# Optimization experiments

Measured on AMD Instinct MI355X. Metric: run time of the kernel, lower is better.

The kernel has to match this reference:

```python
import jax, jax.numpy as jnp
import numpy as np
import math

VOCAB = 50000; D = 512; DEPTH = 6; N = 16; DCONV = 4; R = 32; DFF = 4 * D
B = 2; L = 1024

# A = -exp(A_log) with A_log = log(arange(1..N)) repeated over D  =>  A[d,n] = -(n+1)
A_CONT = -jnp.broadcast_to(jnp.arange(1.0, N + 1, dtype=jnp.float32), (D, N))


def sinusoidal(t, dim):
    half = dim // 2
    f = jnp.exp(jnp.arange(half, dtype=jnp.float32) * (-math.log(10000.0) / (half - 1)))
    e = t.astype(jnp.float32)[:, None] * f[None, :]
    return jnp.concatenate([jnp.sin(e), jnp.cos(e)], axis=-1)


def layernorm(x, g, b, eps=1e-5):
    mu = jnp.mean(x, -1, keepdims=True)
    var = jnp.mean((x - mu) ** 2, -1, keepdims=True)
    return (x - mu) * jax.lax.rsqrt(var + eps) * g + b


def ssm(x, Win, Wconv, Wdt, bdt, Dp, Wout):
    # x: [B,L,D]
    proj = x @ Win.T  # [B,L,2D+R+2N]
    xc, z, dtu, Bp, Cp = jnp.split(proj, [D, 2 * D, 2 * D + R, 2 * D + R + N], axis=-1)
    # depthwise causal conv (left pad d_conv-1 == pad both + truncate to L)
    conv = jax.lax.conv_general_dilated(
        xc.transpose(0, 2, 1), Wconv, (1,), [(DCONV - 1, 0)],
        dimension_numbers=('NCH', 'OIH', 'NCH'), feature_group_count=D)
    u = jax.nn.silu(conv.transpose(0, 2, 1))  # [B,L,D]
    dt = jax.nn.softplus(dtu @ Wdt.T + bdt)   # [B,L,D]
    At = jnp.exp(dt[..., None] * A_CONT)      # [B,L,D,N] (ZOH)
    Bu = ((At - 1.0) / (A_CONT + 1e-10)) * Bp[:, :, None, :] * u[..., None]  # [B,L,D,N]

    def step(h, xs):
        a, bu, c = xs
        h = a * h + bu                       # [B,D,N]
        return h, jnp.einsum('bn,bdn->bd', c, h)

    h0 = jnp.zeros((x.shape[0], D, N), dtype=x.dtype)
    _, ys = jax.lax.scan(step, h0, (At.transpose(1, 0, 2, 3), Bu.transpose(1, 0, 2, 3), Cp.transpose(1, 0, 2)))
    y = ys.transpose(1, 0, 2)                # [B,L,D]
    y = (y + u * Dp) * jax.nn.silu(z)
    return y @ Wout.T


def setup_inputs():
    key = jax.random.key(0)
    ks = iter(jax.random.split(key, 32))
    nrm = lambda shape: jax.random.normal(next(ks), shape, jnp.float32) * 0.02
    inp = {
        'x_t': jax.random.randint(next(ks), (B, L), 0, VOCAB + 1),
        't': jax.random.randint(next(ks), (B,), 0, 100),
        'tok_emb': nrm((VOCAB + 1, D)),
        'tmlp_w1': nrm((4 * D, D)), 'tmlp_b1': jnp.zeros((4 * D,)),
        'tmlp_w2': nrm((D, 4 * D)), 'tmlp_b2': jnp.zeros((D,)),
        'ln1_g': jnp.ones((DEPTH, D)), 'ln1_b': jnp.zeros((DEPTH, D)),
        'in_w': nrm((DEPTH, 2 * D + R + 2 * N, D)),
        'conv_w': nrm((DEPTH, D, 1, DCONV)),
        'dt_w': nrm((DEPTH, D, R)), 'dt_b': jnp.zeros((DEPTH, D)),
        'D_p': jnp.ones((DEPTH, D)),
        'out_w': nrm((DEPTH, D, D)),
        'ln2_g': jnp.ones((DEPTH, D)), 'ln2_b': jnp.zeros((DEPTH, D)),
        'mlp_w1': nrm((DEPTH, DFF, D)), 'mlp_b1': jnp.zeros((DEPTH, DFF)),
        'mlp_w2': nrm((DEPTH, D, DFF)), 'mlp_b2': jnp.zeros((DEPTH, D)),
        'lno_g': jnp.ones((D,)), 'lno_b': jnp.zeros((D,)),
        'head_w': nrm((VOCAB, D)), 'head_b': jnp.zeros((VOCAB,)),
    }
    return inp


def reference(x_t, t, tok_emb, tmlp_w1, tmlp_b1, tmlp_w2, tmlp_b2,
              ln1_g, ln1_b, in_w, conv_w, dt_w, dt_b, D_p, out_w,
              ln2_g, ln2_b, mlp_w1, mlp_b1, mlp_w2, mlp_b2,
              lno_g, lno_b, head_w, head_b):
    te = sinusoidal(t, D)
    te = jax.nn.silu(te @ tmlp_w1.T + tmlp_b1) @ tmlp_w2.T + tmlp_b2  # [B,D]
    x = tok_emb[x_t] + te[:, None, :]                                  # [B,L,D]
    for i in range(DEPTH):
        x = x + ssm(layernorm(x, ln1_g[i], ln1_b[i]),
                    in_w[i], conv_w[i], dt_w[i], dt_b[i], D_p[i], out_w[i])
        h = layernorm(x, ln2_g[i], ln2_b[i])
        x = x + jax.nn.gelu(h @ mlp_w1[i].T + mlp_b1[i], approximate=False) @ mlp_w2[i].T + mlp_b2[i]
    x = layernorm(x, lno_g, lno_b)
    return x @ head_w.T + head_b  # [B,L,VOCAB]
```

## Files before the change

### kernel.cpp

```cpp
#include <hip/hip_runtime.h>
#include <hip/hip_bf16.h>
#include <math.h>

typedef __hip_bfloat16 bf16;
typedef short s16x8 __attribute__((ext_vector_type(8)));
typedef float f32x4 __attribute__((ext_vector_type(4)));

#define M_TOK 2048
#define DD    512
#define LSEQ  1024
#define PW    1088
#define NST   16
#define RR    32
#define DFFW  2048
#define NCH   64
#define CH    16

__device__ __forceinline__ float bf2f(bf16 v) { return __bfloat162float(v); }
__device__ __forceinline__ float siluf(float x) { return x / (1.f + expf(-x)); }

__constant__ float c_invn[NST] = {
  -1.f/1, -1.f/2, -1.f/3, -1.f/4, -1.f/5, -1.f/6, -1.f/7, -1.f/8,
  -1.f/9, -1.f/10, -1.f/11, -1.f/12, -1.f/13, -1.f/14, -1.f/15, -1.f/16 };

__global__ __launch_bounds__(256) void k_te1(
    const int* __restrict__ t, const float* __restrict__ w1, const float* __restrict__ b1,
    float* __restrict__ h1)
{
  __shared__ float semb[2][512];
  int tid = threadIdx.x;
  float t0 = (float)t[0], t1 = (float)t[1];
  {
    int k = tid;
    float f = expf((float)k * (-9.210340371976184f / 255.f));
    semb[0][k]       = sinf(t0 * f);
    semb[0][k + 256] = cosf(t0 * f);
    semb[1][k]       = sinf(t1 * f);
    semb[1][k + 256] = cosf(t1 * f);
  }
  __syncthreads();
  int wave = tid >> 6, lane = tid & 63;
  int j = blockIdx.x * 4 + wave;
  const float* wr = w1 + (size_t)j * 512;
  float s0 = 0.f, s1 = 0.f;
#pragma unroll
  for (int i = 0; i < 8; ++i) {
    int k = lane + (i << 6);
    float wv = wr[k];
    s0 += wv * semb[0][k];
    s1 += wv * semb[1][k];
  }
  for (int o = 32; o; o >>= 1) { s0 += __shfl_down(s0, o); s1 += __shfl_down(s1, o); }
  if (!lane) {
    float bv = b1[j];
    h1[j]        = siluf(s0 + bv);
    h1[2048 + j] = siluf(s1 + bv);
  }
}

__global__ __launch_bounds__(256) void k_te2(
    const float* __restrict__ h1, const float* __restrict__ w2, const float* __restrict__ b2,
    float* __restrict__ te)
{
  __shared__ float sh1[2][2048];
  int tid = threadIdx.x;
  for (int idx = tid; idx < 4096; idx += 256)
    sh1[idx >> 11][idx & 2047] = h1[idx];
  __syncthreads();
  int wave = tid >> 6, lane = tid & 63;
  int d = blockIdx.x * 4 + wave;
  const float* wr = w2 + (size_t)d * 2048;
  float s0 = 0.f, s1 = 0.f;
#pragma unroll
  for (int i = 0; i < 32; ++i) {
    int k = lane + (i << 6);
    float wv = wr[k];
    s0 += wv * sh1[0][k];
    s1 += wv * sh1[1][k];
  }
  for (int o = 32; o; o >>= 1) { s0 += __shfl_down(s0, o); s1 += __shfl_down(s1, o); }
  if (!lane) {
    float bv = b2[d];
    te[d]       = s0 + bv;
    te[512 + d] = s1 + bv;
  }
}

__global__ __launch_bounds__(256) void k_embed(
    const int* __restrict__ x_t, const float* __restrict__ tok,
    const float* __restrict__ te, float* __restrict__ x)
{
  int m = blockIdx.x;
  int b = m >> 10;
  int row = x_t[m];
  const float* src = tok + (size_t)row * DD;
  for (int d = threadIdx.x; d < DD; d += 256)
    x[(size_t)m * DD + d] = src[d] + te[b * DD + d];
}

__global__ __launch_bounds__(256) void k_layernorm(
    const float* __restrict__ x, const float* __restrict__ g, const float* __restrict__ bb,
    bf16* __restrict__ out)
{
  int m = blockIdx.x;
  const float* xr = x + (size_t)m * DD;
  float2 v = ((const float2*)xr)[threadIdx.x];
  float s = v.x + v.y, ss = v.x * v.x + v.y * v.y;
  for (int o = 32; o; o >>= 1) { s += __shfl_down(s, o); ss += __shfl_down(ss, o); }
  __shared__ float ps[4], pss[4];
  int wave = threadIdx.x >> 6, lane = threadIdx.x & 63;
  if (!lane) { ps[wave] = s; pss[wave] = ss; }
  __syncthreads();
  s = ps[0] + ps[1] + ps[2] + ps[3];
  ss = pss[0] + pss[1] + pss[2] + pss[3];
  float mu = s * (1.f / DD);
  float var = ss * (1.f / DD) - mu * mu;
  float inv = rsqrtf(var + 1e-5f);
  int d = threadIdx.x * 2;
  out[(size_t)m * DD + d]     = __float2bfloat16((v.x - mu) * inv * g[d]     + bb[d]);
  out[(size_t)m * DD + d + 1] = __float2bfloat16((v.y - mu) * inv * g[d + 1] + bb[d + 1]);
}

__global__ __launch_bounds__(256) void k_conv_dt(
    const float* __restrict__ proj, const float* __restrict__ convw,
    const float* __restrict__ dtw, const float* __restrict__ dtb,
    float* __restrict__ u, float* __restrict__ dt)
{
  int m = blockIdx.x >> 1;
  int d = ((blockIdx.x & 1) << 8) + threadIdx.x;
  int b = m >> 10, l = m & 1023;
  __shared__ float dtu[RR];
  if (threadIdx.x < RR) dtu[threadIdx.x] = proj[(size_t)m * PW + 2 * DD + threadIdx.x];
  __syncthreads();
  float c = 0.f;
#pragma unroll
  for (int j = 0; j < 4; ++j) {
    int ll = l - 3 + j;
    if (ll >= 0) c += proj[(size_t)(b * LSEQ + ll) * PW + d] * convw[d * 4 + j];
  }
  u[(size_t)m * DD + d] = siluf(c);
  float s = dtb[d];
  const float* wr = dtw + (size_t)d * RR;
#pragma unroll
  for (int r = 0; r < RR; ++r) s += dtu[r] * wr[r];
  dt[(size_t)m * DD + d] = (s > 0.f) ? (s + log1pf(expf(-s))) : log1pf(expf(s));
}

__global__ __launch_bounds__(128) void k_scan1(
    const float* __restrict__ proj, const float* __restrict__ u,
    const float* __restrict__ dt, float* __restrict__ yloc,
    float* __restrict__ Ebuf, float* __restrict__ Aprod, float* __restrict__ hend)
{
  int d = (blockIdx.x << 7) + threadIdx.x;
  int c = blockIdx.y, b = blockIdx.z;
  int m0 = b * LSEQ + c * CH;
  __shared__ float sBC[CH][32];
  for (int idx = threadIdx.x; idx < CH * 32; idx += 128)
    sBC[idx >> 5][idx & 31] = proj[(size_t)(m0 + (idx >> 5)) * PW + 2 * DD + RR + (idx & 31)];
  __syncthreads();
  float h[NST];
#pragma unroll
  for (int n = 0; n < NST; ++n) h[n] = 0.f;
  float S = 0.f;
  for (int l = 0; l < CH; ++l) {
    size_t m = (size_t)(m0 + l);
    float dtv = dt[m * DD + d];
    float uv  = u[m * DD + d];
    float e1 = expf(-dtv);
    S += dtv;
    Ebuf[m * DD + d] = expf(-S);
    float p = 1.f, acc = 0.f;
#pragma unroll
    for (int n = 0; n < NST; ++n) {
      p *= e1;
      float bu = (p - 1.f) * c_invn[n] * sBC[l][n] * uv;
      h[n] = p * h[n] + bu;
      acc += sBC[l][16 + n] * h[n];
    }
    yloc[m * DD + d] = acc;
  }
  float Ec = expf(-S);
  float p = 1.f;
  size_t base = ((size_t)(b * NCH + c) * NST) * DD + d;
#pragma unroll
  for (int n = 0; n < NST; ++n) {
    p *= Ec;
    Aprod[base + (size_t)n * DD] = p;
    hend [base + (size_t)n * DD] = h[n];
  }
}

__global__ __launch_bounds__(256) void k_scan2(
    const float* __restrict__ Aprod, const float* __restrict__ hend, float* __restrict__ h0)
{
  int idx = blockIdx.x * 256 + threadIdx.x;
  int d = idx & 511;
  int n = (idx >> 9) & 15;
  int b = idx >> 13;
  float h = 0.f;
  for (int c = 0; c < NCH; ++c) {
    size_t o = ((size_t)((b * NCH + c) * NST + n)) * DD + d;
    h0[o] = h;
    h = Aprod[o] * h + hend[o];
  }
}

__global__ __launch_bounds__(128) void k_scan3(
    const float* __restrict__ proj, const float* __restrict__ u,
    const float* __restrict__ yloc, const float* __restrict__ Ebuf,
    const float* __restrict__ h0, const float* __restrict__ Dp, bf16* __restrict__ out)
{
  int d = (blockIdx.x << 7) + threadIdx.x;
  int c = blockIdx.y, b = blockIdx.z;
  int m0 = b * LSEQ + c * CH;
  __shared__ float sC[CH][NST];
  for (int idx = threadIdx.x; idx < CH * NST; idx += 128)
    sC[idx >> 4][idx & 15] = proj[(size_t)(m0 + (idx >> 4)) * PW + 2 * DD + RR + NST + (idx & 15)];
  __syncthreads();
  float hh[NST];
  size_t base = ((size_t)(b * NCH + c) * NST) * DD + d;
#pragma unroll
  for (int n = 0; n < NST; ++n) hh[n] = h0[base + (size_t)n * DD];
  float dpv = Dp[d];
  for (int l = 0; l < CH; ++l) {
    size_t m = (size_t)(m0 + l);
    float E = Ebuf[m * DD + d];
    float p = 1.f, corr = 0.f;
#pragma unroll
    for (int n = 0; n < NST; ++n) {
      p *= E;
      corr += sC[l][n] * p * hh[n];
    }
    float y = yloc[m * DD + d] + corr;
    float z = proj[m * PW + DD + d];
    float v = (y + u[m * DD + d] * dpv) * siluf(z);
    out[m * DD + d] = __float2bfloat16(v);
  }
}

template<int ACT, bool BF16OUT, bool RES, bool BIAS, bool TRANS>
__global__ __launch_bounds__(256) void gemm_abt(
    const bf16* __restrict__ A, const float* __restrict__ B,
    const float* __restrict__ bias, const float* __restrict__ res,
    void* __restrict__ Cout, int N, int K)
{
  __shared__ bf16 sA[128][40];
  __shared__ bf16 sB[128][40];
  int bn = (TRANS ? blockIdx.y : blockIdx.x) * 128;
  int bm = (TRANS ? blockIdx.x : blockIdx.y) * 128;
  int tid = threadIdx.x;
  int wave = tid >> 6, lane = tid & 63;
  int wm = (wave >> 1) << 6, wn = (wave & 1) << 6;
  int r = lane & 15, q = lane >> 4;
  int ldr = tid >> 2;
  int ldc = (tid & 3) << 3;

  f32x4 acc[4][4];
#pragma unroll
  for (int i = 0; i < 4; ++i)
#pragma unroll
    for (int j = 0; j < 4; ++j) acc[i][j] = (f32x4){0.f, 0.f, 0.f, 0.f};

  s16x8 pa[2];
  f32x4 pb[2][2];
#define GLOAD(k0)                                                              \
  {                                                                            \
    _Pragma("unroll")                                                          \
    for (int h = 0; h < 2; ++h) {                                              \
      int row = ldr + (h << 6);                                                \
      pa[h] = *(const s16x8*)(A + (size_t)(bm + row) * K + (k0) + ldc);        \
      int nrow = bn + row;                                                     \
      if (nrow < N) {                                                          \
        const float* src = B + (size_t)nrow * K + (k0) + ldc;                  \
        pb[h][0] = *(const f32x4*)src;                                         \
        pb[h][1] = *(const f32x4*)(src + 4);                                   \
      } else {                                                                 \
        pb[h][0] = (f32x4){0.f,0.f,0.f,0.f};                                   \
        pb[h][1] = (f32x4){0.f,0.f,0.f,0.f};                                   \
      }                                                                        \
    }                                                                          \
  }

  GLOAD(0);
  for (int k0 = 0; k0 < K; k0 += 32) {
#pragma unroll
    for (int h = 0; h < 2; ++h) {
      int row = ldr + (h << 6);
      *(s16x8*)&sA[row][ldc] = pa[h];
      bf16* dst = &sB[row][ldc];
      dst[0] = __float2bfloat16(pb[h][0][0]); dst[1] = __float2bfloat16(pb[h][0][1]);
      dst[2] = __float2bfloat16(pb[h][0][2]); dst[3] = __float2bfloat16(pb[h][0][3]);
      dst[4] = __float2bfloat16(pb[h][1][0]); dst[5] = __float2bfloat16(pb[h][1][1]);
      dst[6] = __float2bfloat16(pb[h][1][2]); dst[7] = __float2bfloat16(pb[h][1][3]);
    }
    __syncthreads();
    if (k0 + 32 < K) GLOAD(k0 + 32);
    s16x8 af[4], bg[4];
#pragma unroll
    for (int i = 0; i < 4; ++i) af[i] = *(s16x8*)&sA[wm + i * 16 + r][q << 3];
#pragma unroll
    for (int j = 0; j < 4; ++j) bg[j] = *(s16x8*)&sB[wn + j * 16 + r][q << 3];
#pragma unroll
    for (int i = 0; i < 4; ++i)
#pragma unroll
      for (int j = 0; j < 4; ++j)
        acc[i][j] = __builtin_amdgcn_mfma_f32_16x16x32_bf16(af[i], bg[j], acc[i][j], 0, 0, 0);
    __syncthreads();
  }
#undef GLOAD

#pragma unroll
  for (int i = 0; i < 4; ++i)
#pragma unroll
    for (int j = 0; j < 4; ++j) {
      int n = bn + wn + j * 16 + r;
      if (n >= N) continue;
#pragma unroll
      for (int e = 0; e < 4; ++e) {
        int m = bm + wm + i * 16 + (q << 2) + e;
        float v = acc[i][j][e];
        if (BIAS) v += bias[n];
        if (ACT == 1) v = 0.5f * v * (1.f + erff(v * 0.70710678118f));
        if (RES) v += res[(size_t)m * N + n];
        if (BF16OUT) ((bf16*)Cout)[(size_t)m * N + n] = __float2bfloat16(v);
        else         ((float*)Cout)[(size_t)m * N + n] = v;
      }
    }
}

template<int ACT, bool BF16OUT, bool RES, bool BIAS>
__global__ __launch_bounds__(256) void gemm64(
    const bf16* __restrict__ A, const float* __restrict__ B,
    const float* __restrict__ bias, const float* __restrict__ res,
    void* __restrict__ Cout, int N, int K)
{
  __shared__ bf16 sA[64][40];
  __shared__ bf16 sB[64][40];
  int bn = blockIdx.x * 64;
  int bm = blockIdx.y * 64;
  int tid = threadIdx.x;
  int wave = tid >> 6, lane = tid & 63;
  int wm = (wave >> 1) << 5, wn = (wave & 1) << 5;
  int r = lane & 15, q = lane >> 4;
  int ldr = tid >> 2;
  int ldc = (tid & 3) << 3;

  f32x4 acc[2][2];
#pragma unroll
  for (int i = 0; i < 2; ++i)
#pragma unroll
    for (int j = 0; j < 2; ++j) acc[i][j] = (f32x4){0.f, 0.f, 0.f, 0.f};

  s16x8 pa;
  f32x4 pb[2];
#define GLOAD64(k0)                                                            \
  {                                                                            \
    pa = *(const s16x8*)(A + (size_t)(bm + ldr) * K + (k0) + ldc);             \
    const float* src = B + (size_t)(bn + ldr) * K + (k0) + ldc;                \
    pb[0] = *(const f32x4*)src;                                                \
    pb[1] = *(const f32x4*)(src + 4);                                          \
  }

  GLOAD64(0);
  for (int k0 = 0; k0 < K; k0 += 32) {
    *(s16x8*)&sA[ldr][ldc] = pa;
    {
      bf16* dst = &sB[ldr][ldc];
      dst[0] = __float2bfloat16(pb[0][0]); dst[1] = __float2bfloat16(pb[0][1]);
      dst[2] = __float2bfloat16(pb[0][2]); dst[3] = __float2bfloat16(pb[0][3]);
      dst[4] = __float2bfloat16(pb[1][0]); dst[5] = __float2bfloat16(pb[1][1]);
      dst[6] = __float2bfloat16(pb[1][2]); dst[7] = __float2bfloat16(pb[1][3]);
    }
    __syncthreads();
    if (k0 + 32 < K) GLOAD64(k0 + 32);
    s16x8 af[2], bg[2];
#pragma unroll
    for (int i = 0; i < 2; ++i) af[i] = *(s16x8*)&sA[wm + i * 16 + r][q << 3];
#pragma unroll
    for (int j = 0; j < 2; ++j) bg[j] = *(s16x8*)&sB[wn + j * 16 + r][q << 3];
#pragma unroll
    for (int i = 0; i < 2; ++i)
#pragma unroll
      for (int j = 0; j < 2; ++j)
        acc[i][j] = __builtin_amdgcn_mfma_f32_16x16x32_bf16(af[i], bg[j], acc[i][j], 0, 0, 0);
    __syncthreads();
  }
#undef GLOAD64

#pragma unroll
  for (int i = 0; i < 2; ++i)
#pragma unroll
    for (int j = 0; j < 2; ++j) {
      int n = bn + wn + j * 16 + r;
#pragma unroll
      for (int e = 0; e < 4; ++e) {
        int m = bm + wm + i * 16 + (q << 2) + e;
        float v = acc[i][j][e];
        if (BIAS) v += bias[n];
        if (ACT == 1) v = 0.5f * v * (1.f + erff(v * 0.70710678118f));
        if (RES) v += res[(size_t)m * N + n];
        if (BF16OUT) ((bf16*)Cout)[(size_t)m * N + n] = __float2bfloat16(v);
        else         ((float*)Cout)[(size_t)m * N + n] = v;
      }
    }
}

extern "C" void kernel_launch(void* const* d_in, const int* in_sizes, int n_in,
                              void* d_out, int out_size, void* d_ws, size_t ws_size,
                              hipStream_t stream) {
  const int*   x_t     = (const int*)d_in[0];
  const int*   t       = (const int*)d_in[1];
  const float* tok_emb = (const float*)d_in[2];
  const float* tmlp_w1 = (const float*)d_in[3];
  const float* tmlp_b1 = (const float*)d_in[4];
  const float* tmlp_w2 = (const float*)d_in[5];
  const float* tmlp_b2 = (const float*)d_in[6];
  const float* ln1_g   = (const float*)d_in[7];
  const float* ln1_b   = (const float*)d_in[8];
  const float* in_w    = (const float*)d_in[9];
  const float* conv_w  = (const float*)d_in[10];
  const float* dt_w    = (const float*)d_in[11];
  const float* dt_b    = (const float*)d_in[12];
  const float* D_p     = (const float*)d_in[13];
  const float* out_w   = (const float*)d_in[14];
  const float* ln2_g   = (const float*)d_in[15];
  const float* ln2_b   = (const float*)d_in[16];
  const float* mlp_w1  = (const float*)d_in[17];
  const float* mlp_b1  = (const float*)d_in[18];
  const float* mlp_w2  = (const float*)d_in[19];
  const float* mlp_b2  = (const float*)d_in[20];
  const float* lno_g   = (const float*)d_in[21];
  const float* lno_b   = (const float*)d_in[22];
  const float* head_w  = (const float*)d_in[23];
  const float* head_b  = (const float*)d_in[24];

  char* w = (char*)d_ws;
  float* te    = (float*)w;  w += 4096;
  float* h1t   = (float*)w;  w += 16384;
  float* x     = (float*)w;  w += (size_t)M_TOK * DD * 4;
  bf16*  aIn   = (bf16*)w;   w += (size_t)M_TOK * DD * 2;
  float* proj  = (float*)w;  w += (size_t)M_TOK * PW * 4;
  float* ubuf  = (float*)w;  w += (size_t)M_TOK * DD * 4;
  float* dtbuf = (float*)w;  w += (size_t)M_TOK * DD * 4;
  float* ybuf  = (float*)w;  w += (size_t)M_TOK * DD * 4;
  float* Ebuf  = (float*)w;  w += (size_t)M_TOK * DD * 4;
  float* Aprod = (float*)w;  w += (size_t)2 * NCH * NST * DD * 4;
  float* hend  = (float*)w;  w += (size_t)2 * NCH * NST * DD * 4;
  float* h0    = (float*)w;  w += (size_t)2 * NCH * NST * DD * 4;
  bf16*  gbuf  = (bf16*)proj;

  k_te1<<<512, 256, 0, stream>>>(t, tmlp_w1, tmlp_b1, h1t);
  k_te2<<<128, 256, 0, stream>>>(h1t, tmlp_w2, tmlp_b2, te);
  k_embed<<<M_TOK, 256, 0, stream>>>(x_t, tok_emb, te, x);

  for (int i = 0; i < 6; ++i) {
    const float* inw_i  = in_w   + (size_t)i * PW * DD;
    const float* cw_i   = conv_w + (size_t)i * DD * 4;
    const float* dtw_i  = dt_w   + (size_t)i * DD * RR;
    const float* dtb_i  = dt_b   + (size_t)i * DD;
    const float* dp_i   = D_p    + (size_t)i * DD;
    const float* ow_i   = out_w  + (size_t)i * DD * DD;
    const float* m1_i   = mlp_w1 + (size_t)i * DFFW * DD;
    const float* m1b_i  = mlp_b1 + (size_t)i * DFFW;
    const float* m2_i   = mlp_w2 + (size_t)i * DD * DFFW;
    const float* m2b_i  = mlp_b2 + (size_t)i * DD;

    k_layernorm<<<M_TOK, 256, 0, stream>>>(x, ln1_g + i * DD, ln1_b + i * DD, aIn);
    gemm64<0,false,false,false><<<dim3(PW / 64, M_TOK / 64), 256, 0, stream>>>(
        aIn, inw_i, nullptr, nullptr, proj, PW, DD);
    k_conv_dt<<<M_TOK * 2, 256, 0, stream>>>(proj, cw_i, dtw_i, dtb_i, ubuf, dtbuf);
    k_scan1<<<dim3(4, NCH, 2), 128, 0, stream>>>(proj, ubuf, dtbuf, ybuf, Ebuf, Aprod, hend);
    k_scan2<<<2 * NST * DD / 256, 256, 0, stream>>>(Aprod, hend, h0);
    k_scan3<<<dim3(4, NCH, 2), 128, 0, stream>>>(proj, ubuf, ybuf, Ebuf, h0, dp_i, aIn);
    gemm64<0,false,true,false><<<dim3(DD / 64, M_TOK / 64), 256, 0, stream>>>(
        aIn, ow_i, nullptr, x, x, DD, DD);
    k_layernorm<<<M_TOK, 256, 0, stream>>>(x, ln2_g + i * DD, ln2_b + i * DD, aIn);
    gemm_abt<1,true,false,true,false><<<dim3(DFFW / 128, M_TOK / 128), 256, 0, stream>>>(
        aIn, m1_i, m1b_i, nullptr, gbuf, DFFW, DD);
    gemm64<0,false,true,true><<<dim3(DD / 64, M_TOK / 64), 256, 0, stream>>>(
        gbuf, m2_i, m2b_i, x, x, DD, DFFW);
  }

  k_layernorm<<<M_TOK, 256, 0, stream>>>(x, lno_g, lno_b, aIn);
  gemm_abt<0,false,false,true,true><<<dim3(M_TOK / 128, (50000 + 127) / 128), 256, 0, stream>>>(
      aIn, head_w, head_b, nullptr, d_out, 50000, DD);
}
```

Measured before the change: 1.272 ms.

## Swizzle head GEMM blocks, vectorize bf16 LDS stores, shrink LDS padding, use gemm64 for MLP1

The vocab head GEMM now remaps its flat block index into eight interleaved groups. The aim is that concurrently running blocks share tiles of A and B in cache. The eight scalar fp32→bf16 stores into shared memory become one packed 8-wide vector store in both GEMM kernels. Shared-memory row padding shrinks from 40 to 36 bf16, which leaves 16-byte fragment reads only 8-byte aligned and may split them or cause bank conflicts. The first MLP projection also switches from the 128×128 tile kernel to the 64×64 tile kernel, giving more blocks but less operand reuse per block.

```diff
diff --git a/kernel.cpp b/kernel.cpp
--- a/kernel.cpp
+++ b/kernel.cpp
@@ -15,9 +15,23 @@
 #define DFFW  2048
 #define NCH   64
 #define CH    16
+#define PAD   36
 
 __device__ __forceinline__ float bf2f(bf16 v) { return __bfloat162float(v); }
 __device__ __forceinline__ float siluf(float x) { return x / (1.f + expf(-x)); }
+
+__device__ __forceinline__ s16x8 cvt8(const f32x4& a, const f32x4& b) {
+  s16x8 r;
+  r[0] = (short)__bfloat16_as_ushort(__float2bfloat16(a[0]));
+  r[1] = (short)__bfloat16_as_ushort(__float2bfloat16(a[1]));
+  r[2] = (short)__bfloat16_as_ushort(__float2bfloat16(a[2]));
+  r[3] = (short)__bfloat16_as_ushort(__float2bfloat16(a[3]));
+  r[4] = (short)__bfloat16_as_ushort(__float2bfloat16(b[0]));
+  r[5] = (short)__bfloat16_as_ushort(__float2bfloat16(b[1]));
+  r[6] = (short)__bfloat16_as_ushort(__float2bfloat16(b[2]));
+  r[7] = (short)__bfloat16_as_ushort(__float2bfloat16(b[3]));
+  return r;
+}
 
 __constant__ float c_invn[NST] = {
   -1.f/1, -1.f/2, -1.f/3, -1.f/4, -1.f/5, -1.f/6, -1.f/7, -1.f/8,
@@ -238,16 +252,25 @@
   }
 }
 
-template<int ACT, bool BF16OUT, bool RES, bool BIAS, bool TRANS>
+template<int ACT, bool BF16OUT, bool RES, bool BIAS, bool SWZ>
 __global__ __launch_bounds__(256) void gemm_abt(
     const bf16* __restrict__ A, const float* __restrict__ B,
     const float* __restrict__ bias, const float* __restrict__ res,
     void* __restrict__ Cout, int N, int K)
 {
-  __shared__ bf16 sA[128][40];
-  __shared__ bf16 sB[128][40];
-  int bn = (TRANS ? blockIdx.y : blockIdx.x) * 128;
-  int bm = (TRANS ? blockIdx.x : blockIdx.y) * 128;
+  __shared__ bf16 sA[128][PAD];
+  __shared__ bf16 sB[128][PAD];
+  int bn, bm;
+  if (SWZ) {
+    int flat = blockIdx.y * gridDim.x + blockIdx.x;
+    int q = (gridDim.x * gridDim.y) >> 3;
+    int s = (flat & 7) * q + (flat >> 3);
+    bm = (s % gridDim.x) * 128;
+    bn = (s / gridDim.x) * 128;
+  } else {
+    bn = blockIdx.x * 128;
+    bm = blockIdx.y * 128;
+  }
   int tid = threadIdx.x;
   int wave = tid >> 6, lane = tid & 63;
   int wm = (wave >> 1) << 6, wn = (wave & 1) << 6;
@@ -287,11 +310,7 @@
     for (int h = 0; h < 2; ++h) {
       int row = ldr + (h << 6);
       *(s16x8*)&sA[row][ldc] = pa[h];
-      bf16* dst = &sB[row][ldc];
-      dst[0] = __float2bfloat16(pb[h][0][0]); dst[1] = __float2bfloat16(pb[h][0][1]);
-      dst[2] = __float2bfloat16(pb[h][0][2]); dst[3] = __float2bfloat16(pb[h][0][3]);
-      dst[4] = __float2bfloat16(pb[h][1][0]); dst[5] = __float2bfloat16(pb[h][1][1]);
-      dst[6] = __float2bfloat16(pb[h][1][2]); dst[7] = __float2bfloat16(pb[h][1][3]);
+      *(s16x8*)&sB[row][ldc] = cvt8(pb[h][0], pb[h][1]);
     }
     __syncthreads();
     if (k0 + 32 < K) GLOAD(k0 + 32);
@@ -334,8 +353,8 @@
     const float* __restrict__ bias, const float* __restrict__ res,
     void* __restrict__ Cout, int N, int K)
 {
-  __shared__ bf16 sA[64][40];
-  __shared__ bf16 sB[64][40];
+  __shared__ bf16 sA[64][PAD];
+  __shared__ bf16 sB[64][PAD];
   int bn = blockIdx.x * 64;
   int bm = blockIdx.y * 64;
   int tid = threadIdx.x;
@@ -364,13 +383,7 @@
   GLOAD64(0);
   for (int k0 = 0; k0 < K; k0 += 32) {
     *(s16x8*)&sA[ldr][ldc] = pa;
-    {
-      bf16* dst = &sB[ldr][ldc];
-      dst[0] = __float2bfloat16(pb[0][0]); dst[1] = __float2bfloat16(pb[0][1]);
-      dst[2] = __float2bfloat16(pb[0][2]); dst[3] = __float2bfloat16(pb[0][3]);
-      dst[4] = __float2bfloat16(pb[1][0]); dst[5] = __float2bfloat16(pb[1][1]);
-      dst[6] = __float2bfloat16(pb[1][2]); dst[7] = __float2bfloat16(pb[1][3]);
-    }
+    *(s16x8*)&sB[ldr][ldc] = cvt8(pb[0], pb[1]);
     __syncthreads();
     if (k0 + 32 < K) GLOAD64(k0 + 32);
     s16x8 af[2], bg[2];
@@ -475,7 +488,7 @@
     gemm64<0,false,true,false><<<dim3(DD / 64, M_TOK / 64), 256, 0, stream>>>(
         aIn, ow_i, nullptr, x, x, DD, DD);
     k_layernorm<<<M_TOK, 256, 0, stream>>>(x, ln2_g + i * DD, ln2_b + i * DD, aIn);
-    gemm_abt<1,true,false,true,false><<<dim3(DFFW / 128, M_TOK / 128), 256, 0, stream>>>(
+    gemm64<1,true,false,true><<<dim3(DFFW / 64, M_TOK / 64), 256, 0, stream>>>(
         aIn, m1_i, m1b_i, nullptr, gbuf, DFFW, DD);
     gemm64<0,false,true,true><<<dim3(DD / 64, M_TOK / 64), 256, 0, stream>>>(
         gbuf, m2_i, m2b_i, x, x, DD, DFFW);
```

After: 1.222 ms. -3.9%, faster.
